# Kernel optimization log

Hardware: AMD Instinct MI355X
Metric: run time of the kernel (lower is better)

## Reference

```python
import jax, jax.numpy as jnp
import numpy as np

K = 16  # number of neighbors (module init arg)

def setup_inputs() -> dict:
    key = jax.random.key(0)
    M, D, N = 65536, 16, 64
    x = jax.random.normal(key, (M, D), dtype=jnp.float32)
    # equal-length segments: each point set has M // N points
    segs = jnp.full((N,), M // N, dtype=jnp.int64)
    return {"x": x, "segs": segs}

def reference(x, segs):
    # Segmented kNN graph. Segments are equal-length (static shapes for jit),
    # so the per-segment pairwise distance + top-k becomes a batched op.
    B = segs.shape[0]
    M, D = x.shape
    L = M // B  # points per segment
    pts = x.reshape(B, L, D)
    # squared euclidean distances within each segment: (B, L, L)
    sq = jnp.sum(pts * pts, axis=-1)
    d2 = sq[:, :, None] + sq[:, None, :] - 2.0 * jnp.einsum('bld,bmd->blm', pts, pts)
    # k smallest distances per point (includes self, as in DGL's knn_graph)
    _, idx = jax.lax.top_k(-d2, K)  # idx: (B, L, K), local indices within segment
    offsets = (jnp.arange(B, dtype=idx.dtype) * L)[:, None, None]
    src = (idx + offsets).reshape(-1)                      # neighbor -> global node id
    dst = (jnp.arange(L, dtype=idx.dtype)[None, :, None] + offsets)  # (B, L, 1)
    dst = jnp.broadcast_to(dst, (B, L, K)).reshape(-1)
    # edges point from k-nearest neighbors (predecessors) to each node
    return src, dst
```

## Files before the change

### kernel.cpp

```cpp
#include <hip/hip_runtime.h>
#include <stdint.h>


#define L_SEG 1024
#define M_PTS 65536

typedef __fp16 fp16x2 __attribute__((ext_vector_type(2)));
typedef __fp16 fp16x4 __attribute__((ext_vector_type(4)));
typedef float  f32x4  __attribute__((ext_vector_type(4)));

__device__ __forceinline__ uint32_t umn(uint32_t a, uint32_t b) { return a < b ? a : b; }
__device__ __forceinline__ uint32_t umx(uint32_t a, uint32_t b) { return a > b ? a : b; }

__device__ __forceinline__ void clean16(uint32_t* A) {
    #pragma unroll
    for (int j = 8; j > 0; j >>= 1) {
        #pragma unroll
        for (int i = 0; i < 16; ++i) {
            int p = i ^ j;
            if (p > i) {
                uint32_t lo = umn(A[i], A[p]);
                uint32_t hi = umx(A[i], A[p]);
                A[i] = lo; A[p] = hi;
            }
        }
    }
}

__global__ __launch_bounds__(256, 4) void knn_v5_kernel(const float* __restrict__ x,
                                                        int* __restrict__ out) {
    __shared__ __attribute__((aligned(16))) __fp16 sc[L_SEG * 16];
    __shared__ __attribute__((aligned(16))) float  ssq[L_SEG];

    const int tid = threadIdx.x;
    const int b   = blockIdx.x;
    const int seg = (b & 7) * 8 + (b >> 7);
    const int qp  = (b >> 3) & 15;
    const float* xseg = x + (size_t)seg * (L_SEG * 16);

    {
        const f32x4* gx  = (const f32x4*)xseg;
        fp16x4*      scv = (fp16x4*)sc;
        #pragma unroll
        for (int i = 0; i < 16; ++i) {
            f32x4 v = gx[tid + 256 * i];
            union { fp16x2 h2[2]; fp16x4 h4; } u;
            u.h2[0] = __builtin_amdgcn_cvt_pkrtz(v[0], v[1]);
            u.h2[1] = __builtin_amdgcn_cvt_pkrtz(v[2], v[3]);
            scv[tid + 256 * i] = u.h4;
        }
    }
    __syncthreads();

    {
        const int r0 = tid << 2;
        #pragma unroll
        for (int c = 0; c < 4; ++c) {
            const fp16x2* hp = (const fp16x2*)(sc + (size_t)(r0 + c) * 16);
            float s = 128.0f;
            #pragma unroll
            for (int j = 0; j < 8; ++j) {
                fp16x2 hh = hp[j];
                float f0 = (float)hh[0], f1 = (float)hh[1];
                s = __builtin_fmaf(f0, f0, s);
                s = __builtin_fmaf(f1, f1, s);
            }
            ssq[r0 + c] = s;
        }
    }
    __syncthreads();

    const int lane = tid & 63;
    const int w    = tid >> 6;
    const int g    = lane >> 4;
    const int col  = lane & 15;
    const int qloc = qp * 64 + w * 16 + col;

    const fp16x4 bfrag = *(const fp16x4*)(sc + (size_t)qloc * 16 + g * 4);

    uint32_t A[16];
    #pragma unroll
    for (int i = 0; i < 16; ++i) A[i] = 0xFFFFFFFFu;

    const __fp16* ap0 = sc + (size_t)col * 16 + g * 4;

    for (int t0 = 0; t0 < 16; ++t0) {
        uint32_t B[16];
        #pragma unroll
        for (int tt = 0; tt < 4; ++tt) {
            const int tb = t0 * 64 + tt * 16;
            fp16x4 af = *(const fp16x4*)(ap0 + (size_t)tb * 16);
            f32x4 z = {0.f, 0.f, 0.f, 0.f};
            f32x4 acc = __builtin_amdgcn_mfma_f32_16x16x16f16(af, bfrag, z, 0, 0, 0);
            const f32x4 sq = *(const f32x4*)&ssq[tb + g * 4];
            const uint32_t idxt = (uint32_t)(tb + g * 4);
            #pragma unroll
            for (int v = 0; v < 4; ++v) {
                float kf = __builtin_fmaf(acc[v], -2.0f, sq[v]);
                B[tt * 4 + v] = (__float_as_uint(kf) & 0xFFFFFC00u) | (idxt + (uint32_t)v);
            }
        }
        #pragma unroll
        for (int p = 1; p < 16; p <<= 1) {
            #pragma unroll
            for (int k = p; k >= 1; k >>= 1) {
                #pragma unroll
                for (int j = (k & (p - 1)); j + k < 16; j += 2 * k) {
                    #pragma unroll
                    for (int i = 0; i <= ((k - 1 < 15 - j - k) ? k - 1 : 15 - j - k); ++i) {
                        if ((i + j) / (2 * p) == (i + j + k) / (2 * p)) {
                            uint32_t lo = umn(B[i + j], B[i + j + k]);
                            uint32_t hi = umx(B[i + j], B[i + j + k]);
                            B[i + j] = lo; B[i + j + k] = hi;
                        }
                    }
                }
            }
        }
        #pragma unroll
        for (int i = 0; i < 16; ++i) A[i] = umn(A[i], B[15 - i]);
        clean16(A);
    }

    #pragma unroll
    for (int m = 16; m <= 32; m <<= 1) {
        uint32_t P[16];
        #pragma unroll
        for (int i = 0; i < 16; ++i) P[i] = (uint32_t)__shfl_xor((int)A[15 - i], m, 64);
        #pragma unroll
        for (int i = 0; i < 16; ++i) A[i] = umn(A[i], P[i]);
        clean16(A);
    }

    const int base = seg * L_SEG;
    const int q    = base + qloc;
    uint32_t r[4];
    #pragma unroll
    for (int v = 0; v < 4; ++v) {
        uint32_t t01 = (g & 1) ? A[4 + v]  : A[v];
        uint32_t t23 = (g & 1) ? A[12 + v] : A[8 + v];
        r[v] = (g & 2) ? t23 : t01;
    }
    int4 sv;
    sv.x = base + (int)(r[0] & 1023u);
    sv.y = base + (int)(r[1] & 1023u);
    sv.z = base + (int)(r[2] & 1023u);
    sv.w = base + (int)(r[3] & 1023u);
    ((int4*)out)[(size_t)q * 4 + g] = sv;
    ((int4*)out)[(size_t)M_PTS * 4 + (size_t)q * 4 + g] = make_int4(q, q, q, q);
}

extern "C" void kernel_launch(void* const* d_in, const int* in_sizes, int n_in,
                              void* d_out, int out_size, void* d_ws, size_t ws_size,
                              hipStream_t stream) {
    const float* x = (const float*)d_in[0];
    int* out = (int*)d_out;
    (void)d_ws; (void)ws_size;
    knn_v5_kernel<<<dim3(1024), dim3(256), 0, stream>>>(x, out);
}
```

Measured before the change: 92.36 us.

## Pre-swizzle candidate fragments in LDS, fold -2 scale and norms into MFMA

Candidate points are now stored in LDS already permuted into MFMA A-fragment order and pre-scaled by -2. Each lane can then fetch two tiles with one 16-byte load, and the next iteration's fragments are prefetched. Squared norms are computed from the fp32 global data and passed as the MFMA accumulator, which removes the per-element FMA. Query fragments get their own small LDS buffer, and the separate norm pass no longer needs a barrier. The cost is scattered global reads during staging and slight precision differences, since the norms now come from fp32 rather than fp16.

```diff
diff --git a/kernel.cpp b/kernel.cpp
--- a/kernel.cpp
+++ b/kernel.cpp
@@ -27,45 +27,65 @@
     }
 }
 
-__global__ __launch_bounds__(256, 4) void knn_v5_kernel(const float* __restrict__ x,
+__global__ __launch_bounds__(256, 4) void knn_v6_kernel(const float* __restrict__ x,
                                                         int* __restrict__ out) {
-    __shared__ __attribute__((aligned(16))) __fp16 sc[L_SEG * 16];
+    __shared__ __attribute__((aligned(16))) __fp16 sfrag[16384];
     __shared__ __attribute__((aligned(16))) float  ssq[L_SEG];
+    __shared__ __attribute__((aligned(16))) __fp16 sq16[64 * 16];
 
     const int tid = threadIdx.x;
     const int b   = blockIdx.x;
     const int seg = (b & 7) * 8 + (b >> 7);
     const int qp  = (b >> 3) & 15;
     const float* xseg = x + (size_t)seg * (L_SEG * 16);
+    const f32x4* gx4  = (const f32x4*)xseg;
 
     {
-        const f32x4* gx  = (const f32x4*)xseg;
-        fp16x4*      scv = (fp16x4*)sc;
+        fp16x4* fr = (fp16x4*)sfrag;
         #pragma unroll
         for (int i = 0; i < 16; ++i) {
-            f32x4 v = gx[tid + 256 * i];
+            const int F    = i * 256 + tid;
+            const int bat  = F >> 8;
+            const int half = (F >> 7) & 1;
+            const int e    = (F >> 1) & 63;
+            const int lo   = F & 1;
+            const int tt   = half * 2 + lo;
+            const int g    = e >> 4;
+            const int col  = e & 15;
+            const int cand = bat * 64 + tt * 16 + col;
+            f32x4 v = gx4[cand * 4 + g];
+            union { fp16x2 h2[2]; fp16x4 h4; } u;
+            u.h2[0] = __builtin_amdgcn_cvt_pkrtz(-2.0f * v[0], -2.0f * v[1]);
+            u.h2[1] = __builtin_amdgcn_cvt_pkrtz(-2.0f * v[2], -2.0f * v[3]);
+            fr[F] = u.h4;
+        }
+    }
+    {
+        const int c0 = tid << 2;
+        #pragma unroll
+        for (int c = 0; c < 4; ++c) {
+            float s = 128.0f;
+            #pragma unroll
+            for (int d = 0; d < 4; ++d) {
+                f32x4 v = gx4[(c0 + c) * 4 + d];
+                s = __builtin_fmaf(v[0], v[0], s);
+                s = __builtin_fmaf(v[1], v[1], s);
+                s = __builtin_fmaf(v[2], v[2], s);
+                s = __builtin_fmaf(v[3], v[3], s);
+            }
+            ssq[c0 + c] = s;
+        }
+    }
+    if (tid < 64) {
+        const f32x4* qg = gx4 + (size_t)(qp * 64 + tid) * 4;
+        fp16x4* dst = (fp16x4*)(sq16 + (size_t)tid * 16);
+        #pragma unroll
+        for (int d = 0; d < 4; ++d) {
+            f32x4 v = qg[d];
             union { fp16x2 h2[2]; fp16x4 h4; } u;
             u.h2[0] = __builtin_amdgcn_cvt_pkrtz(v[0], v[1]);
             u.h2[1] = __builtin_amdgcn_cvt_pkrtz(v[2], v[3]);
-            scv[tid + 256 * i] = u.h4;
-        }
-    }
-    __syncthreads();
-
-    {
-        const int r0 = tid << 2;
-        #pragma unroll
-        for (int c = 0; c < 4; ++c) {
-            const fp16x2* hp = (const fp16x2*)(sc + (size_t)(r0 + c) * 16);
-            float s = 128.0f;
-            #pragma unroll
-            for (int j = 0; j < 8; ++j) {
-                fp16x2 hh = hp[j];
-                float f0 = (float)hh[0], f1 = (float)hh[1];
-                s = __builtin_fmaf(f0, f0, s);
-                s = __builtin_fmaf(f1, f1, s);
-            }
-            ssq[r0 + c] = s;
+            dst[d] = u.h4;
         }
     }
     __syncthreads();
@@ -76,29 +96,37 @@
     const int col  = lane & 15;
     const int qloc = qp * 64 + w * 16 + col;
 
-    const fp16x4 bfrag = *(const fp16x4*)(sc + (size_t)qloc * 16 + g * 4);
+    const fp16x4 bfrag = *(const fp16x4*)(sq16 + (size_t)(w * 16 + col) * 16 + g * 4);
 
     uint32_t A[16];
     #pragma unroll
     for (int i = 0; i < 16; ++i) A[i] = 0xFFFFFFFFu;
 
-    const __fp16* ap0 = sc + (size_t)col * 16 + g * 4;
+    const char* fb = (const char*)sfrag;
+    const int   lb = lane * 16;
+
+    union F2H { f32x4 v; fp16x4 h[2]; };
+    F2H cur01, cur23;
+    cur01.v = *(const f32x4*)(fb + lb);
+    cur23.v = *(const f32x4*)(fb + 1024 + lb);
 
     for (int t0 = 0; t0 < 16; ++t0) {
+        const int nb = ((t0 + 1) & 15) * 2048;
+        F2H nxt01, nxt23;
+        nxt01.v = *(const f32x4*)(fb + nb + lb);
+        nxt23.v = *(const f32x4*)(fb + nb + 1024 + lb);
+
         uint32_t B[16];
         #pragma unroll
         for (int tt = 0; tt < 4; ++tt) {
             const int tb = t0 * 64 + tt * 16;
-            fp16x4 af = *(const fp16x4*)(ap0 + (size_t)tb * 16);
-            f32x4 z = {0.f, 0.f, 0.f, 0.f};
-            f32x4 acc = __builtin_amdgcn_mfma_f32_16x16x16f16(af, bfrag, z, 0, 0, 0);
             const f32x4 sq = *(const f32x4*)&ssq[tb + g * 4];
+            fp16x4 af = (tt < 2) ? cur01.h[tt] : cur23.h[tt - 2];
+            f32x4 acc = __builtin_amdgcn_mfma_f32_16x16x16f16(af, bfrag, sq, 0, 0, 0);
             const uint32_t idxt = (uint32_t)(tb + g * 4);
             #pragma unroll
-            for (int v = 0; v < 4; ++v) {
-                float kf = __builtin_fmaf(acc[v], -2.0f, sq[v]);
-                B[tt * 4 + v] = (__float_as_uint(kf) & 0xFFFFFC00u) | (idxt + (uint32_t)v);
-            }
+            for (int v = 0; v < 4; ++v)
+                B[tt * 4 + v] = (__float_as_uint(acc[v]) & 0xFFFFFC00u) | (idxt + (uint32_t)v);
         }
         #pragma unroll
         for (int p = 1; p < 16; p <<= 1) {
@@ -120,6 +148,8 @@
         #pragma unroll
         for (int i = 0; i < 16; ++i) A[i] = umn(A[i], B[15 - i]);
         clean16(A);
+
+        cur01 = nxt01; cur23 = nxt23;
     }
 
     #pragma unroll
@@ -156,5 +186,5 @@
     const float* x = (const float*)d_in[0];
     int* out = (int*)d_out;
     (void)d_ws; (void)ws_size;
-    knn_v5_kernel<<<dim3(1024), dim3(256), 0, stream>>>(x, out);
+    knn_v6_kernel<<<dim3(1024), dim3(256), 0, stream>>>(x, out);
 }
```

Result: no change. 92.05 us (-0.3%).
